# Optimization experiments

Hardware: AMD Instinct MI355X
Metric: run time of the kernel (lower is better)

## Reference

```python
import jax, jax.numpy as jnp
import numpy as np

N_NODES = 1_000_000   # nodal points, 3 DOFs each
N_ELEMS = 500_000     # H8 (8-node hexahedral) elements
N_TYPES = 64          # distinct element stiffness matrices (24x24)


def setup_inputs() -> dict:
    key = jax.random.key(0)
    k1, k2, k3, k4 = jax.random.split(key, 4)
    U = jax.random.normal(k1, (N_NODES, 3), dtype=jnp.float32)
    filters = jax.random.normal(k2, (N_TYPES, 24, 24), dtype=jnp.float32)
    H8types = jax.random.randint(k3, (N_ELEMS,), 0, N_TYPES, dtype=jnp.int32)
    nodIdx = jax.random.randint(k4, (N_ELEMS, 8), 0, N_NODES, dtype=jnp.int32)
    return {"U": U, "filters": filters, "H8types": H8types, "nodIdx": nodIdx}


def reference(U, filters, H8types, nodIdx):
    """FEM stiffness matvec KU = sum_e scatter(K_type(e) @ gather(U, e)).

    U:       [N, 3]      nodal displacements (3 DOFs per node)
    filters: [T, 24, 24] per-type element stiffness matrices
    H8types: [E]         element type index into filters
    nodIdx:  [E, 8]      element -> node connectivity
    returns KU: [N, 3]
    """
    E = nodIdx.shape[0]
    # gather the 8 nodes x 3 DOFs of each element -> [E, 24]
    ue = U[nodIdx].reshape(E, 24)
    # per-type stiffness for each element -> [E, 24, 24]
    Ke = filters[H8types]
    # per-element force vector f_e = K_e @ u_e -> [E, 24]
    fe = jnp.einsum('eij,ej->ei', Ke, ue)
    # scatter-add element forces back to nodal DOFs
    KU = jnp.zeros_like(U).at[nodIdx.reshape(-1)].add(fe.reshape(E * 8, 3))
    return KU
```

## Files before the change

kernel.cpp:

```cpp
#include <hip/hip_runtime.h>


#define NTYPES    64
#define KSTRIDE   580
#define RSHIFT    11
#define RNODES    2048
#define MAXB      512
#define CAP       10240
#define K1_TPB    1024
#define K2_TPB    512

typedef int          nint4  __attribute__((ext_vector_type(4)));
typedef unsigned int nuint4 __attribute__((ext_vector_type(4)));


__global__ __launch_bounds__(K1_TPB, 1) void feconv_bin_kernel(
    const float* __restrict__ U,
    const float* __restrict__ K,
    const int*   __restrict__ types,
    const int*   __restrict__ nodIdx,
    float*       __restrict__ KU,
    unsigned*    __restrict__ tails,
    nuint4*      __restrict__ recs,
    int n_elems, int n_buckets)
{
    extern __shared__ float sK[];
    __shared__ unsigned sCnt[MAXB];
    __shared__ unsigned sBase[MAXB];

    for (int w = threadIdx.x; w < NTYPES * 576; w += K1_TPB) {
        int t = w / 576;
        int r = w - t * 576;
        sK[t * KSTRIDE + r] = K[w];
    }
    for (int i = threadIdx.x; i < n_buckets; i += K1_TPB) sCnt[i] = 0;
    __syncthreads();

    const int e = blockIdx.x * K1_TPB + threadIdx.x;
    int nodes[8];
    int tt = -1;

    if (e < n_elems) {
        tt = __builtin_nontemporal_load(&types[e]);
        const nint4* q = (const nint4*)(nodIdx + (size_t)e * 8);
        nint4 a = __builtin_nontemporal_load(q);
        nint4 b = __builtin_nontemporal_load(q + 1);
        nodes[0] = a.x; nodes[1] = a.y; nodes[2] = a.z; nodes[3] = a.w;
        nodes[4] = b.x; nodes[5] = b.y; nodes[6] = b.z; nodes[7] = b.w;
#pragma unroll
        for (int j = 0; j < 8; ++j)
            atomicAdd(&sCnt[(unsigned)nodes[j] >> RSHIFT], 1u);
    }
    __syncthreads();

    for (int b = threadIdx.x; b < n_buckets; b += K1_TPB) {
        unsigned c = sCnt[b];
        sBase[b] = c ? atomicAdd(&tails[b], c) : 0u;
        sCnt[b] = 0;
    }
    __syncthreads();

    if (tt >= 0) {
        float ue[24];
#pragma unroll
        for (int j = 0; j < 8; ++j) {
            const float* up = U + (size_t)nodes[j] * 3;
            ue[3 * j + 0] = up[0];
            ue[3 * j + 1] = up[1];
            ue[3 * j + 2] = up[2];
        }

        const float4* Kt4 = (const float4*)(sK + tt * KSTRIDE);
#pragma unroll
        for (int j = 0; j < 8; ++j) {
            float a0 = 0.f, a1 = 0.f, a2 = 0.f;
#pragma unroll
            for (int q = 0; q < 6; ++q) {
                float4 k0 = Kt4[(3 * j + 0) * 6 + q];
                float4 k1 = Kt4[(3 * j + 1) * 6 + q];
                float4 k2 = Kt4[(3 * j + 2) * 6 + q];
                float u0 = ue[4 * q + 0], u1 = ue[4 * q + 1];
                float u2 = ue[4 * q + 2], u3 = ue[4 * q + 3];
                a0 += k0.x * u0 + k0.y * u1 + k0.z * u2 + k0.w * u3;
                a1 += k1.x * u0 + k1.y * u1 + k1.z * u2 + k1.w * u3;
                a2 += k2.x * u0 + k2.y * u1 + k2.z * u2 + k2.w * u3;
            }
            unsigned n = (unsigned)nodes[j];
            unsigned b = n >> RSHIFT;
            unsigned pos = sBase[b] + atomicAdd(&sCnt[b], 1u);
            if (pos < CAP) {
                nuint4 r = { n, __float_as_uint(a0),
                             __float_as_uint(a1), __float_as_uint(a2) };
                recs[(size_t)b * CAP + pos] = r;
            } else {
                atomicAdd(&KU[(size_t)n * 3 + 0], a0);
                atomicAdd(&KU[(size_t)n * 3 + 1], a1);
                atomicAdd(&KU[(size_t)n * 3 + 2], a2);
            }
        }
    }
}


__global__ __launch_bounds__(K2_TPB) void feconv_acc_kernel(
    const nuint4*   __restrict__ recs,
    const unsigned* __restrict__ tails,
    float*          __restrict__ KU,
    int n_nodes)
{
    __shared__ float sAcc[RNODES * 3];
    const int b = blockIdx.x;

    for (int i = threadIdx.x; i < RNODES * 3; i += K2_TPB) sAcc[i] = 0.f;
    __syncthreads();

    unsigned cnt = tails[b];
    if (cnt > CAP) cnt = CAP;
    const nuint4* base = recs + (size_t)b * CAP;
    for (unsigned i = threadIdx.x; i < cnt; i += K2_TPB) {
        nuint4 r = base[i];
        unsigned local = (r.x & (RNODES - 1)) * 3;
        atomicAdd(&sAcc[local + 0], __uint_as_float(r.y));
        atomicAdd(&sAcc[local + 1], __uint_as_float(r.z));
        atomicAdd(&sAcc[local + 2], __uint_as_float(r.w));
    }
    __syncthreads();

    const int nbase = b * RNODES;
    int limit = n_nodes - nbase;
    if (limit > RNODES) limit = RNODES;
    limit *= 3;
    float* out = KU + (size_t)nbase * 3;
    for (int i = threadIdx.x; i < limit; i += K2_TPB) out[i] += sAcc[i];
}


__global__ __launch_bounds__(256) void feconv_elem_kernel(
    const float* __restrict__ U, const float* __restrict__ K,
    const int* __restrict__ types, const int* __restrict__ nodIdx,
    float* __restrict__ KU, int n_elems)
{
    int e = blockIdx.x * blockDim.x + threadIdx.x;
    if (e >= n_elems) return;
    int t = types[e];
    const int4* idx4 = (const int4*)(nodIdx + (size_t)e * 8);
    int4 iA = idx4[0], iB = idx4[1];
    int nodes[8] = {iA.x, iA.y, iA.z, iA.w, iB.x, iB.y, iB.z, iB.w};
    float ue[24];
#pragma unroll
    for (int j = 0; j < 8; ++j) {
        const float* up = U + (size_t)nodes[j] * 3;
        ue[3 * j + 0] = up[0]; ue[3 * j + 1] = up[1]; ue[3 * j + 2] = up[2];
    }
    const float* Kt = K + (size_t)t * 576;
#pragma unroll
    for (int i = 0; i < 24; ++i) {
        const float4* row = (const float4*)(Kt + i * 24);
        float acc = 0.f;
#pragma unroll
        for (int q = 0; q < 6; ++q) {
            float4 k = row[q];
            acc += k.x * ue[4 * q + 0] + k.y * ue[4 * q + 1]
                 + k.z * ue[4 * q + 2] + k.w * ue[4 * q + 3];
        }
        atomicAdd(&KU[(size_t)nodes[i / 3] * 3 + (i % 3)], acc);
    }
}

extern "C" void kernel_launch(void* const* d_in, const int* in_sizes, int n_in,
                              void* d_out, int out_size, void* d_ws, size_t ws_size,
                              hipStream_t stream) {
    const float* U      = (const float*)d_in[0];
    const float* Kf     = (const float*)d_in[1];
    const int*   types  = (const int*)d_in[2];
    const int*   nodIdx = (const int*)d_in[3];
    float*       KU     = (float*)d_out;

    const int n_elems = in_sizes[2];
    const int n_nodes = in_sizes[0] / 3;
    const int n_buckets = (n_nodes + RNODES - 1) / RNODES;

    (void)hipMemsetAsync(KU, 0, (size_t)out_size * sizeof(float), stream);

    const size_t rec_off = 4096;
    const size_t need    = rec_off + (size_t)n_buckets * CAP * sizeof(nuint4);

    if (n_buckets <= MAXB && ws_size >= need) {
        unsigned* tails = (unsigned*)d_ws;
        nuint4*   recs  = (nuint4*)((char*)d_ws + rec_off);

        (void)hipMemsetAsync(tails, 0, 4096, stream);

        size_t lds_bytes = (size_t)NTYPES * KSTRIDE * sizeof(float);
        int grid1 = (n_elems + K1_TPB - 1) / K1_TPB;
        feconv_bin_kernel<<<grid1, K1_TPB, lds_bytes, stream>>>(
            U, Kf, types, nodIdx, KU, tails, recs, n_elems, n_buckets);
        feconv_acc_kernel<<<n_buckets, K2_TPB, 0, stream>>>(
            recs, tails, KU, n_nodes);
    } else {
        int block = 256;
        int grid = (n_elems + block - 1) / block;
        feconv_elem_kernel<<<grid, block, 0, stream>>>(
            U, Kf, types, nodIdx, KU, n_elems);
    }
}
```

Measured before the change: 240.2 us.

## Pack U to bf16 and shrink scatter records to 12 bytes with embedded index

Adds a pre-pass that converts U to bf16, packed into 8 bytes per node, so the random gathers in the binning kernel fetch one 8-byte word instead of three floats. Scatter records drop from 16 to 12 bytes by hiding the 11-bit local node index in the low mantissa bits of the three force values. Both aim to cut memory traffic in the gather and scatter phases. In exchange, the displacement inputs and the element forces lose precision, which risks tolerance failures, and the extra pack kernel adds a full pass over U.

```diff
diff --git a/kernel.cpp b/kernel.cpp
--- a/kernel.cpp
+++ b/kernel.cpp
@@ -9,19 +9,39 @@
 #define CAP       10240
 #define K1_TPB    1024
 #define K2_TPB    512
+#define PREP_TPB  256
 
 typedef int          nint4  __attribute__((ext_vector_type(4)));
-typedef unsigned int nuint4 __attribute__((ext_vector_type(4)));
+typedef unsigned int nuint2 __attribute__((ext_vector_type(2)));
+
+__device__ __forceinline__ unsigned bf16_rne(float f) {
+    unsigned b = __float_as_uint(f);
+    return (b + 0x7FFFu + ((b >> 16) & 1u)) >> 16;
+}
+
+
+__global__ __launch_bounds__(PREP_TPB) void pack_u_kernel(
+    const float* __restrict__ U, nuint2* __restrict__ Ub, int n_nodes)
+{
+    int n = blockIdx.x * PREP_TPB + threadIdx.x;
+    if (n >= n_nodes) return;
+    const float* up = U + (size_t)n * 3;
+    unsigned bx = bf16_rne(up[0]);
+    unsigned by = bf16_rne(up[1]);
+    unsigned bz = bf16_rne(up[2]);
+    nuint2 v = { bx | (by << 16), bz };
+    Ub[n] = v;
+}
 
 
 __global__ __launch_bounds__(K1_TPB, 1) void feconv_bin_kernel(
-    const float* __restrict__ U,
+    const nuint2* __restrict__ Ub,
     const float* __restrict__ K,
     const int*   __restrict__ types,
     const int*   __restrict__ nodIdx,
     float*       __restrict__ KU,
     unsigned*    __restrict__ tails,
-    nuint4*      __restrict__ recs,
+    unsigned*    __restrict__ recs,
     int n_elems, int n_buckets)
 {
     extern __shared__ float sK[];
@@ -64,10 +84,10 @@
         float ue[24];
 #pragma unroll
         for (int j = 0; j < 8; ++j) {
-            const float* up = U + (size_t)nodes[j] * 3;
-            ue[3 * j + 0] = up[0];
-            ue[3 * j + 1] = up[1];
-            ue[3 * j + 2] = up[2];
+            nuint2 v = Ub[nodes[j]];
+            ue[3 * j + 0] = __uint_as_float(v.x << 16);
+            ue[3 * j + 1] = __uint_as_float(v.x & 0xFFFF0000u);
+            ue[3 * j + 2] = __uint_as_float(v.y << 16);
         }
 
         const float4* Kt4 = (const float4*)(sK + tt * KSTRIDE);
@@ -89,9 +109,11 @@
             unsigned b = n >> RSHIFT;
             unsigned pos = sBase[b] + atomicAdd(&sCnt[b], 1u);
             if (pos < CAP) {
-                nuint4 r = { n, __float_as_uint(a0),
-                             __float_as_uint(a1), __float_as_uint(a2) };
-                recs[(size_t)b * CAP + pos] = r;
+                unsigned local = n & (RNODES - 1);
+                size_t base = 3 * ((size_t)b * CAP + pos);
+                recs[base + 0] = (__float_as_uint(a0) & ~15u) | (local & 15u);
+                recs[base + 1] = (__float_as_uint(a1) & ~15u) | ((local >> 4) & 15u);
+                recs[base + 2] = (__float_as_uint(a2) & ~15u) | (local >> 8);
             } else {
                 atomicAdd(&KU[(size_t)n * 3 + 0], a0);
                 atomicAdd(&KU[(size_t)n * 3 + 1], a1);
@@ -103,7 +125,7 @@
 
 
 __global__ __launch_bounds__(K2_TPB) void feconv_acc_kernel(
-    const nuint4*   __restrict__ recs,
+    const unsigned* __restrict__ recs,
     const unsigned* __restrict__ tails,
     float*          __restrict__ KU,
     int n_nodes)
@@ -116,13 +138,16 @@
 
     unsigned cnt = tails[b];
     if (cnt > CAP) cnt = CAP;
-    const nuint4* base = recs + (size_t)b * CAP;
+    const unsigned* base = recs + 3 * ((size_t)b * CAP);
     for (unsigned i = threadIdx.x; i < cnt; i += K2_TPB) {
-        nuint4 r = base[i];
-        unsigned local = (r.x & (RNODES - 1)) * 3;
-        atomicAdd(&sAcc[local + 0], __uint_as_float(r.y));
-        atomicAdd(&sAcc[local + 1], __uint_as_float(r.z));
-        atomicAdd(&sAcc[local + 2], __uint_as_float(r.w));
+        unsigned w0 = base[3 * i + 0];
+        unsigned w1 = base[3 * i + 1];
+        unsigned w2 = base[3 * i + 2];
+        unsigned local = (w0 & 15u) | ((w1 & 15u) << 4) | ((w2 & 7u) << 8);
+        unsigned o = local * 3;
+        atomicAdd(&sAcc[o + 0], __uint_as_float(w0 & ~15u));
+        atomicAdd(&sAcc[o + 1], __uint_as_float(w1 & ~15u));
+        atomicAdd(&sAcc[o + 2], __uint_as_float(w2 & ~15u));
     }
     __syncthreads();
 
@@ -182,19 +207,24 @@
 
     (void)hipMemsetAsync(KU, 0, (size_t)out_size * sizeof(float), stream);
 
-    const size_t rec_off = 4096;
-    const size_t need    = rec_off + (size_t)n_buckets * CAP * sizeof(nuint4);
+    const size_t ub_off  = 4096;
+    const size_t rec_off = ub_off + (((size_t)n_nodes * 8 + 255) & ~255ull);
+    const size_t need    = rec_off + (size_t)n_buckets * CAP * 12;
 
     if (n_buckets <= MAXB && ws_size >= need) {
         unsigned* tails = (unsigned*)d_ws;
-        nuint4*   recs  = (nuint4*)((char*)d_ws + rec_off);
+        nuint2*   Ub    = (nuint2*)((char*)d_ws + ub_off);
+        unsigned* recs  = (unsigned*)((char*)d_ws + rec_off);
 
         (void)hipMemsetAsync(tails, 0, 4096, stream);
+
+        int gridP = (n_nodes + PREP_TPB - 1) / PREP_TPB;
+        pack_u_kernel<<<gridP, PREP_TPB, 0, stream>>>(U, Ub, n_nodes);
 
         size_t lds_bytes = (size_t)NTYPES * KSTRIDE * sizeof(float);
         int grid1 = (n_elems + K1_TPB - 1) / K1_TPB;
         feconv_bin_kernel<<<grid1, K1_TPB, lds_bytes, stream>>>(
-            U, Kf, types, nodIdx, KU, tails, recs, n_elems, n_buckets);
+            Ub, Kf, types, nodIdx, KU, tails, recs, n_elems, n_buckets);
         feconv_acc_kernel<<<n_buckets, K2_TPB, 0, stream>>>(
             recs, tails, KU, n_nodes);
     } else {
```

Result: no change. 237.9 us (-0.9%).
